# Optimization experiments

Measured on AMD Instinct MI355X. Metric: run time of the kernel, lower is better.

## Reference

```python
import jax, jax.numpy as jnp
import numpy as np

N = 10000   # num_nodes (batch=1)
E = 160000  # num edges
CIN, H, T, OUT, K = 32, 64, 12, 12, 3


def _conv1d(x, w, b, pad):
    # x: [N, C_in, T], w: [C_out, C_in, K]
    out = jax.lax.conv_general_dilated(
        x, w, window_strides=(1,), padding=[(pad, pad)],
        dimension_numbers=('NCH', 'OIH', 'NCH'))
    return out + b[None, :, None]


def _gated_tconv(x, w, b):
    # GatedTemporalConv (dropout = identity in eval)
    out = _conv1d(x, w, b, K // 2)
    P, Q = jnp.split(out, 2, axis=1)
    return P * jax.nn.sigmoid(Q)


def _gcn(x, W, b, src, dst, ew):
    # PyG GCNConv, vectorized over all T timesteps in one fused pass.
    # x: [N, C_in, T], W: [C_out, C_in]
    xt = jnp.einsum('nct,oc->not', x, W)
    loop = jnp.arange(N)
    srcl = jnp.concatenate([src, loop])
    dstl = jnp.concatenate([dst, loop])
    ewl = jnp.concatenate([ew, jnp.ones((N,), ew.dtype)])
    deg = jax.ops.segment_sum(ewl, dstl, num_segments=N)
    dis = jnp.where(deg > 0, jax.lax.rsqrt(deg), 0.0)
    norm = dis[srcl] * ewl * dis[dstl]                      # [E+N]
    msg = xt[srcl] * norm[:, None, None]                    # [E+N, C_out, T]
    out = jax.ops.segment_sum(msg, dstl, num_segments=N)    # [N, C_out, T]
    return out + b[None, :, None]


def setup_inputs() -> dict:
    key = jax.random.key(0)
    ks = jax.random.split(key, 20)
    rn = lambda k, s: jax.random.normal(k, s, jnp.float32) * 0.05
    return {
        'x': jax.random.normal(ks[0], (N, CIN, T), jnp.float32),
        'edge_index': jax.random.randint(ks[1], (2, E), 0, N),
        'edge_weight': jax.random.uniform(ks[2], (E,), jnp.float32),
        'tc1a_w': rn(ks[3], (2 * H, CIN, K)), 'tc1a_b': rn(ks[4], (2 * H,)),
        'gc1_w': rn(ks[5], (H, H)),           'gc1_b': rn(ks[6], (H,)),
        'tc1b_w': rn(ks[7], (2 * H, H, K)),   'tc1b_b': rn(ks[8], (2 * H,)),
        'tc2a_w': rn(ks[9], (2 * H, H, K)),   'tc2a_b': rn(ks[10], (2 * H,)),
        'gc2_w': rn(ks[11], (H, H)),          'gc2_b': rn(ks[12], (H,)),
        'tc2b_w': rn(ks[13], (2 * H, H, K)),  'tc2b_b': rn(ks[14], (2 * H,)),
        'fin_w': rn(ks[15], (OUT, H, T)),     'fin_b': rn(ks[16], (OUT,)),
    }


def reference(x, edge_index, edge_weight,
              tc1a_w, tc1a_b, gc1_w, gc1_b, tc1b_w, tc1b_b,
              tc2a_w, tc2a_b, gc2_w, gc2_b, tc2b_w, tc2b_b,
              fin_w, fin_b):
    src, dst = edge_index[0], edge_index[1]
    h = _gated_tconv(x, tc1a_w, tc1a_b)
    h = jax.nn.relu(_gcn(h, gc1_w, gc1_b, src, dst, edge_weight))
    h = _gated_tconv(h, tc1b_w, tc1b_b)
    h = _gated_tconv(h, tc2a_w, tc2a_b)
    h = jax.nn.relu(_gcn(h, gc2_w, gc2_b, src, dst, edge_weight))
    h = _gated_tconv(h, tc2b_w, tc2b_b)
    h = _conv1d(h, fin_w, fin_b, 0)          # [N, OUT, 1] (kernel == T)
    h = h[:, :, 0]                            # squeeze(-1)
    return h.reshape(1, N, OUT)               # batch_size = 1
```

## Files before the change

### kernel.cpp

```cpp
#include <hip/hip_runtime.h>
#include <hip/hip_bf16.h>
#include <stdint.h>

#define N_NODES 10000
#define N_EDGES 160000
#define BUCKET 128
#define UNROLL_SLOTS 24

typedef unsigned short u16;
typedef unsigned int u32;
typedef short s16v8 __attribute__((ext_vector_type(8)));
typedef float f32v4 __attribute__((ext_vector_type(4)));
typedef float f32v2 __attribute__((ext_vector_type(2)));
typedef unsigned int u32v4 __attribute__((ext_vector_type(4)));
typedef unsigned int u32v2 __attribute__((ext_vector_type(2)));

__device__ __forceinline__ float bf2f(u16 v){ return __uint_as_float(((u32)v) << 16); }
__device__ __forceinline__ u16 f2bf(float f){
    u32 u = __float_as_uint(f);
    u32 r = (u + 0x7fffu + ((u >> 16) & 1u)) >> 16;
    return (u16)r;
}
__device__ __forceinline__ f32v2 up2(u32 v){
    f32v2 r;
    r.x = __uint_as_float(v << 16);
    r.y = __uint_as_float(v & 0xffff0000u);
    return r;
}
__device__ __forceinline__ u32 pk2(float lo, float hi){
    return (u32)f2bf(lo) | ((u32)f2bf(hi) << 16);
}

struct SmallPtrs { const void* p[14]; };

__device__ __constant__ const int g_seg_off[15] = {
    0, 12288, 12416, 16512, 16576, 41152, 41280,
    65856, 65984, 70080, 70144, 94720, 94848, 104064, 104076
};
__device__ __constant__ const int g_seg_kind[14] = {
    1, 0, 0, 0, 2, 0, 2, 0, 0, 0, 2, 0, 0, 0
};

__global__ void k_convert_init(SmallPtrs ps, u16* __restrict__ dst,
                               float* deg, int* cur){
    int i = blockIdx.x * blockDim.x + threadIdx.x;
    if (i < 104076){
        int seg = 0, base = 0;
#pragma unroll
        for (int s = 0; s < 14; s++){
            if (i >= g_seg_off[s]){ seg = s; base = g_seg_off[s]; }
        }
        int li = i - base;
        float v = ((const float*)ps.p[seg])[li];
        int kind = g_seg_kind[seg];
        int dsto = li;
        if (kind){
            int CIN = (kind == 1) ? 32 : 64;
            int o = li / (3 * CIN);
            int rem = li - o * (3 * CIN);
            int c = rem / 3, d = rem - c * 3;
            dsto = d * 128 * CIN + o * CIN + c;
        }
        dst[base + dsto] = f2bf(v);
    }
    if (i < N_NODES){ deg[i] = 1.0f; cur[i] = 0; }
}

__launch_bounds__(256, 4)
__global__ void k_gconv_count(const float* __restrict__ xin, const u16* __restrict__ wg,
                              const u16* __restrict__ bg, u16* __restrict__ out,
                              const int* __restrict__ ei, const float* __restrict__ ew,
                              float* deg, int* cur, int2* __restrict__ epack){
    if (blockIdx.x >= 1250){
        int e = (blockIdx.x - 1250) * 256 + threadIdx.x;
        if (e < N_EDGES){
            int s = ei[e];
            int d = ei[N_EDGES + e];
            float wv = ew[e];
            atomicAdd(&deg[d], wv);
            int p = atomicAdd(&cur[d], 1);
            if (p < BUCKET) epack[d * BUCKET + p] = make_int2(s, __float_as_int(wv));
        }
        return;
    }
    __shared__ __attribute__((aligned(16))) u16 shbuf[6912];
    u16* xT = shbuf;
    u16* Ho = shbuf;
    int tid = threadIdx.x;
    int n0 = blockIdx.x * 8;

    int lane = tid & 63, wave = tid >> 6;
    int col = lane & 15, quad = lane >> 4;
    int o_p = wave * 16 + col, o_q = o_p + 64;

    s16v8 Bf[3][2];
#pragma unroll
    for (int pq = 0; pq < 2; pq++){
        int o = pq ? o_q : o_p;
#pragma unroll
        for (int d = 0; d < 3; d++)
            Bf[d][pq] = *(const s16v8*)(wg + d * 4096 + o * 32 + quad * 8);
    }

    for (int i = tid; i < 8 * 40; i += 256){
        int g = i / 40, c = i % 40;
        xT[g * 560 + 0 * 40 + c] = 0; xT[g * 560 + 13 * 40 + c] = 0;
    }
    {
        int g = tid >> 5, c = tid & 31;
        const float4* p = (const float4*)(xin + ((size_t)(n0 + g) * 32 + c) * 12);
        float4 v0 = p[0], v1 = p[1], v2 = p[2];
        u16* xb = xT + g * 560 + c;
        xb[1 * 40] = f2bf(v0.x);  xb[2 * 40] = f2bf(v0.y);
        xb[3 * 40] = f2bf(v0.z);  xb[4 * 40] = f2bf(v0.w);
        xb[5 * 40] = f2bf(v1.x);  xb[6 * 40] = f2bf(v1.y);
        xb[7 * 40] = f2bf(v1.z);  xb[8 * 40] = f2bf(v1.w);
        xb[9 * 40] = f2bf(v2.x);  xb[10 * 40] = f2bf(v2.y);
        xb[11 * 40] = f2bf(v2.z); xb[12 * 40] = f2bf(v2.w);
    }
    __syncthreads();

    f32v4 aP[6], aQ[6];
#pragma unroll
    for (int mt = 0; mt < 6; mt++){ aP[mt] = (f32v4)0.f; aQ[mt] = (f32v4)0.f; }
#pragma unroll
    for (int mt = 0; mt < 6; mt++){
        int m = mt * 16 + col;
        int g = m / 12, t = m - 12 * g;
#pragma unroll
        for (int d = 0; d < 3; d++){
            s16v8 a = *(const s16v8*)&xT[g * 560 + (t + d) * 40 + quad * 8];
            aP[mt] = __builtin_amdgcn_mfma_f32_16x16x32_bf16(a, Bf[d][0], aP[mt], 0, 0, 0);
            aQ[mt] = __builtin_amdgcn_mfma_f32_16x16x32_bf16(a, Bf[d][1], aQ[mt], 0, 0, 0);
        }
    }
    __syncthreads();
    float bP = bf2f(bg[o_p]), bQ = bf2f(bg[o_q]);
#pragma unroll
    for (int mt = 0; mt < 6; mt++){
#pragma unroll
        for (int r = 0; r < 4; r++){
            int m2 = mt * 16 + quad * 4 + r;
            int g = m2 / 12, t = m2 - 12 * g;
            float pv = aP[mt][r] + bP, qv = aQ[mt][r] + bQ;
            Ho[g * 864 + t * 72 + o_p] = f2bf(pv / (1.f + __expf(-qv)));
        }
    }
    __syncthreads();
    for (int i = tid; i < 768; i += 256){
        int g = i / 96, r = i % 96, t = r / 8, ch = r % 8;
        *(s16v8*)(out + (size_t)(n0 + g) * 768 + t * 64 + ch * 8) =
            *(const s16v8*)&Ho[g * 864 + t * 72 + ch * 8];
    }
}

__global__ void k_norm(const float* __restrict__ deg, const int* __restrict__ cur,
                       int2* __restrict__ ep){
    int i = blockIdx.x * blockDim.x + threadIdx.x;
    int n = i >> 7, slot = i & 127;
    if (n >= N_NODES) return;
    int cnt = cur[n]; if (cnt > BUCKET) cnt = BUCKET;
    if (slot < cnt){
        int2 e = ep[(size_t)n * BUCKET + slot];
        float w = __int_as_float(e.y) * rsqrtf(deg[e.x]) * rsqrtf(deg[n]);
        ep[(size_t)n * BUCKET + slot].y = __float_as_int(w);
    } else if (slot < UNROLL_SLOTS){
        ep[(size_t)n * BUCKET + slot] = make_int2(0, 0);
    }
}

#define GATHER2(P) { \
    int4 m = *(const int4*)(eb + (P)); \
    const u16* q0 = src + (size_t)(u32)m.x * 768; \
    const u16* q1 = src + (size_t)(u32)m.z * 768; \
    u32v4 a0 = *(const u32v4*)(q0 + off1); u32v2 b0 = *(const u32v2*)(q0 + off2); \
    u32v4 a1 = *(const u32v4*)(q1 + off1); u32v2 b1 = *(const u32v2*)(q1 + off2); \
    f32v2 w0; w0.x = __int_as_float(m.y); w0.y = w0.x; \
    f32v2 w1; w1.x = __int_as_float(m.w); w1.y = w1.x; \
    acc[0] += w0 * up2(a0.x); acc[1] += w0 * up2(a0.y); \
    acc[2] += w0 * up2(a0.z); acc[3] += w0 * up2(a0.w); \
    acc[4] += w0 * up2(b0.x); acc[5] += w0 * up2(b0.y); \
    acc[0] += w1 * up2(a1.x); acc[1] += w1 * up2(a1.y); \
    acc[2] += w1 * up2(a1.z); acc[3] += w1 * up2(a1.w); \
    acc[4] += w1 * up2(b1.x); acc[5] += w1 * up2(b1.y); }

#define GATHER1(P) { \
    int2 e0 = eb[(P)]; \
    const u16* q0 = src + (size_t)(u32)e0.x * 768; \
    u32v4 a0 = *(const u32v4*)(q0 + off1); u32v2 b0 = *(const u32v2*)(q0 + off2); \
    f32v2 w0; w0.x = __int_as_float(e0.y); w0.y = w0.x; \
    acc[0] += w0 * up2(a0.x); acc[1] += w0 * up2(a0.y); \
    acc[2] += w0 * up2(a0.z); acc[3] += w0 * up2(a0.w); \
    acc[4] += w0 * up2(b0.x); acc[5] += w0 * up2(b0.y); }

__launch_bounds__(256, 8)
__global__ void k_gather(const u16* __restrict__ src, const float* __restrict__ deg,
                         const int* __restrict__ cur, const int2* __restrict__ ep,
                         u16* __restrict__ z){
    int slice = blockIdx.x & 7;
    int nb = blockIdx.x >> 3;
    int tid = threadIdx.x;
    int nl = tid >> 5;
    int sub = tid & 31;
    int eg = sub >> 3;
    int l8 = sub & 7;
    int n = nb * 8 + nl;
    int off1 = slice * 96 + l8 * 8;
    int off2 = slice * 96 + 64 + l8 * 4;

    int e = cur[n]; if (e > BUCKET) e = BUCKET;

    f32v2 acc[6];
    if (eg == 0){
        float sw = 1.0f / deg[n];
        f32v2 swv; swv.x = sw; swv.y = sw;
        const u16* xr = src + (size_t)n * 768;
        u32v4 sa = *(const u32v4*)(xr + off1);
        u32v2 sb = *(const u32v2*)(xr + off2);
        acc[0] = swv * up2(sa.x); acc[1] = swv * up2(sa.y);
        acc[2] = swv * up2(sa.z); acc[3] = swv * up2(sa.w);
        acc[4] = swv * up2(sb.x); acc[5] = swv * up2(sb.y);
    } else {
#pragma unroll
        for (int k = 0; k < 6; k++) acc[k] = (f32v2)0.f;
    }

    const int2* eb = ep + (size_t)n * BUCKET;
    GATHER2(eg * 2);
    GATHER2(eg * 2 + 8);
    GATHER2(eg * 2 + 16);

    if (e > UNROLL_SLOTS){
        int p = UNROLL_SLOTS + eg * 2;
        for (; p + 1 < e; p += 8) GATHER2(p);
        if (p < e) GATHER1(p);
    }

    float r[12];
#pragma unroll
    for (int j = 0; j < 6; j++){ r[2 * j] = acc[j].x; r[2 * j + 1] = acc[j].y; }
#pragma unroll
    for (int k = 0; k < 12; k++){
        r[k] += __shfl_xor(r[k], 8, 64);
        r[k] += __shfl_xor(r[k], 16, 64);
    }
    if (eg == 0){
        u16* zo = z + (size_t)n * 768;
        u32v4 ha; ha.x = pk2(r[0], r[1]); ha.y = pk2(r[2], r[3]);
        ha.z = pk2(r[4], r[5]); ha.w = pk2(r[6], r[7]);
        u32v2 hb; hb.x = pk2(r[8], r[9]); hb.y = pk2(r[10], r[11]);
        *(u32v4*)(zo + off1) = ha;
        *(u32v2*)(zo + off2) = hb;
    }
}

#define XIDX(g, row, c) (((g) * 14 + (row)) * 72 + (c))

template<bool LAST>
__launch_bounds__(256, 4)
__global__ void k_fused(const u16* __restrict__ z,
                        const u16* __restrict__ Wmix, const u16* __restrict__ bmix,
                        const u16* __restrict__ w1, const u16* __restrict__ b1,
                        const u16* __restrict__ w2, const u16* __restrict__ b2,
                        const u16* __restrict__ fw, const u16* __restrict__ fb,
                        u16* __restrict__ outMid, float* __restrict__ outFin){
    __shared__ __attribute__((aligned(16))) u16 bufX[8 * 14 * 72];
    __shared__ __attribute__((aligned(16))) u16 bufY[8 * 14 * 72];
    int tid = threadIdx.x;
    int n0 = blockIdx.x * 8;
    int lane = tid & 63, wave = tid >> 6;
    int col = lane & 15, quad = lane >> 4;
    int o_p = wave * 16 + col, o_q = o_p + 64;

    for (int i = tid; i < 8 * 72; i += 256){
        int g = i / 72, c = i % 72;
        bufX[XIDX(g, 0, c)] = 0; bufX[XIDX(g, 13, c)] = 0;
        bufY[XIDX(g, 0, c)] = 0; bufY[XIDX(g, 13, c)] = 0;
    }
    for (int i = tid; i < 768; i += 256){
        int g = i / 96, r = i % 96, t = r >> 3, ch = r & 7;
        *(s16v8*)&bufX[XIDX(g, 1 + t, ch * 8)] =
            *(const s16v8*)(z + (size_t)(n0 + g) * 768 + t * 64 + ch * 8);
    }
    __syncthreads();

    {
        f32v4 accm[6];
#pragma unroll
        for (int mt = 0; mt < 6; mt++) accm[mt] = (f32v4)0.f;
#pragma unroll
        for (int ks = 0; ks < 2; ks++){
            s16v8 Bm = *(const s16v8*)(Wmix + (size_t)o_p * 64 + ks * 32 + quad * 8);
#pragma unroll
            for (int mt = 0; mt < 6; mt++){
                int m = mt * 16 + col;
                int g = m / 12, t = m - 12 * g;
                s16v8 a = *(const s16v8*)&bufX[XIDX(g, 1 + t, ks * 32 + quad * 8)];
                accm[mt] = __builtin_amdgcn_mfma_f32_16x16x32_bf16(a, Bm, accm[mt], 0, 0, 0);
            }
        }
        float bm = bf2f(bmix[o_p]);
#pragma unroll
        for (int mt = 0; mt < 6; mt++){
#pragma unroll
            for (int r = 0; r < 4; r++){
                int m2 = mt * 16 + quad * 4 + r;
                int g = m2 / 12, t = m2 - 12 * g;
                bufY[XIDX(g, 1 + t, o_p)] = f2bf(fmaxf(accm[mt][r] + bm, 0.f));
            }
        }
    }
    __syncthreads();

    {
        f32v4 aP[6], aQ[6];
#pragma unroll
        for (int mt = 0; mt < 6; mt++){ aP[mt] = (f32v4)0.f; aQ[mt] = (f32v4)0.f; }
#pragma unroll
        for (int ks = 0; ks < 2; ks++){
            s16v8 Bf[3][2];
#pragma unroll
            for (int pq = 0; pq < 2; pq++){
                int o = pq ? o_q : o_p;
#pragma unroll
                for (int d = 0; d < 3; d++)
                    Bf[d][pq] = *(const s16v8*)(w1 + d * 8192 + o * 64 + ks * 32 + quad * 8);
            }
#pragma unroll
            for (int mt = 0; mt < 6; mt++){
                int m = mt * 16 + col;
                int g = m / 12, t = m - 12 * g;
#pragma unroll
                for (int d = 0; d < 3; d++){
                    s16v8 a = *(const s16v8*)&bufY[XIDX(g, t + d, ks * 32 + quad * 8)];
                    aP[mt] = __builtin_amdgcn_mfma_f32_16x16x32_bf16(a, Bf[d][0], aP[mt], 0, 0, 0);
                    aQ[mt] = __builtin_amdgcn_mfma_f32_16x16x32_bf16(a, Bf[d][1], aQ[mt], 0, 0, 0);
                }
            }
        }
        float bP = bf2f(b1[o_p]), bQ = bf2f(b1[o_q]);
#pragma unroll
        for (int mt = 0; mt < 6; mt++){
#pragma unroll
            for (int r = 0; r < 4; r++){
                int m2 = mt * 16 + quad * 4 + r;
                int g = m2 / 12, t = m2 - 12 * g;
                float pv = aP[mt][r] + bP, qv = aQ[mt][r] + bQ;
                u16 hv = f2bf(pv / (1.f + __expf(-qv)));
                if (LAST) bufX[g * 1008 + o_p * 12 + t] = hv;
                else      bufX[XIDX(g, 1 + t, o_p)] = hv;
            }
        }
    }
    __syncthreads();

    if (!LAST){
        f32v4 aP[6], aQ[6];
#pragma unroll
        for (int mt = 0; mt < 6; mt++){ aP[mt] = (f32v4)0.f; aQ[mt] = (f32v4)0.f; }
#pragma unroll
        for (int ks = 0; ks < 2; ks++){
            s16v8 Bf[3][2];
#pragma unroll
            for (int pq = 0; pq < 2; pq++){
                int o = pq ? o_q : o_p;
#pragma unroll
                for (int d = 0; d < 3; d++)
                    Bf[d][pq] = *(const s16v8*)(w2 + d * 8192 + o * 64 + ks * 32 + quad * 8);
            }
#pragma unroll
            for (int mt = 0; mt < 6; mt++){
                int m = mt * 16 + col;
                int g = m / 12, t = m - 12 * g;
#pragma unroll
                for (int d = 0; d < 3; d++){
                    s16v8 a = *(const s16v8*)&bufX[XIDX(g, t + d, ks * 32 + quad * 8)];
                    aP[mt] = __builtin_amdgcn_mfma_f32_16x16x32_bf16(a, Bf[d][0], aP[mt], 0, 0, 0);
                    aQ[mt] = __builtin_amdgcn_mfma_f32_16x16x32_bf16(a, Bf[d][1], aQ[mt], 0, 0, 0);
                }
            }
        }
        float bP = bf2f(b2[o_p]), bQ = bf2f(b2[o_q]);
#pragma unroll
        for (int mt = 0; mt < 6; mt++){
#pragma unroll
            for (int r = 0; r < 4; r++){
                int m2 = mt * 16 + quad * 4 + r;
                int g = m2 / 12, t = m2 - 12 * g;
                float pv = aP[mt][r] + bP, qv = aQ[mt][r] + bQ;
                bufY[XIDX(g, 1 + t, o_p)] = f2bf(pv / (1.f + __expf(-qv)));
            }
        }
        __syncthreads();
        for (int i = tid; i < 768; i += 256){
            int g = i / 96, r = i % 96, t = r / 8, ch = r % 8;
            *(s16v8*)(outMid + (size_t)(n0 + g) * 768 + t * 64 + ch * 8) =
                *(const s16v8*)&bufY[XIDX(g, 1 + t, ch * 8)];
        }
    } else {
        if (wave == 0){
            f32v4 accF = {0.f, 0.f, 0.f, 0.f};
            int g8 = col & 7;
#pragma unroll
            for (int ks = 0; ks < 24; ks++){
                s16v8 a = *(const s16v8*)&bufX[g8 * 1008 + ks * 32 + quad * 8];
                s16v8 bfr = {0, 0, 0, 0, 0, 0, 0, 0};
                if (col < 12)
                    bfr = *(const s16v8*)(fw + (size_t)col * 768 + ks * 32 + quad * 8);
                accF = __builtin_amdgcn_mfma_f32_16x16x32_bf16(a, bfr, accF, 0, 0, 0);
            }
            if (col < 12 && quad < 2){
                float bb = bf2f(fb[col]);
#pragma unroll
                for (int r = 0; r < 4; r++){
                    int g = quad * 4 + r;
                    outFin[(size_t)(n0 + g) * 12 + col] = accF[r] + bb;
                }
            }
        }
    }
}

static inline size_t align256(size_t x){ return (x + 255) & ~(size_t)255; }

extern "C" void kernel_launch(void* const* d_in, const int* in_sizes, int n_in,
                              void* d_out, int out_size, void* d_ws, size_t ws_size,
                              hipStream_t stream){
    const float* x  = (const float*)d_in[0];
    const int* ei   = (const int*)d_in[1];
    const float* ew = (const float*)d_in[2];

    char* w = (char*)d_ws;
    u16* bufA    = (u16*)w;  w += align256((size_t)N_NODES * 768 * sizeof(u16));
    u16* bufB    = (u16*)w;  w += align256((size_t)N_NODES * 768 * sizeof(u16));
    u16* zA      = (u16*)w;  w += align256((size_t)N_NODES * 768 * sizeof(u16));
    u16* zB      = (u16*)w;  w += align256((size_t)N_NODES * 768 * sizeof(u16));
    float* deg   = (float*)w; w += align256(N_NODES * sizeof(float));
    int* cur     = (int*)w;   w += align256(N_NODES * sizeof(int));
    int2* epack  = (int2*)w;  w += align256((size_t)N_NODES * BUCKET * sizeof(int2));
    u16* cvt     = (u16*)w;   w += align256(104076 * sizeof(u16));

    u16* tc1a_w = cvt + 0;
    u16* tc1a_b = cvt + 12288;
    u16* gc1_w  = cvt + 12416;
    u16* gc1_b  = cvt + 16512;
    u16* tc1b_w = cvt + 16576;
    u16* tc1b_b = cvt + 41152;
    u16* tc2a_w = cvt + 41280;
    u16* tc2a_b = cvt + 65856;
    u16* gc2_w  = cvt + 65984;
    u16* gc2_b  = cvt + 70080;
    u16* tc2b_w = cvt + 70144;
    u16* tc2b_b = cvt + 94720;
    u16* fin_w  = cvt + 94848;
    u16* fin_b  = cvt + 104064;

    SmallPtrs ps;
    ps.p[0]  = d_in[3];  ps.p[1]  = d_in[4];
    ps.p[2]  = d_in[5];  ps.p[3]  = d_in[6];
    ps.p[4]  = d_in[7];  ps.p[5]  = d_in[8];
    ps.p[6]  = d_in[9];  ps.p[7]  = d_in[10];
    ps.p[8]  = d_in[11]; ps.p[9]  = d_in[12];
    ps.p[10] = d_in[13]; ps.p[11] = d_in[14];
    ps.p[12] = d_in[15]; ps.p[13] = d_in[16];

    k_convert_init<<<(104076 + 255) / 256, 256, 0, stream>>>(ps, cvt, deg, cur);
    k_gconv_count<<<1250 + 625, 256, 0, stream>>>(x, tc1a_w, tc1a_b, bufA, ei, ew, deg, cur, epack);
    k_norm<<<(N_NODES * BUCKET) / 256, 256, 0, stream>>>(deg, cur, epack);

    k_gather<<<1250 * 8, 256, 0, stream>>>(bufA, deg, cur, epack, zA);
    k_fused<false><<<1250, 256, 0, stream>>>(zA, gc1_w, gc1_b, tc1b_w, tc1b_b,
                                             tc2a_w, tc2a_b, nullptr, nullptr,
                                             bufB, nullptr);
    k_gather<<<1250 * 8, 256, 0, stream>>>(bufB, deg, cur, epack, zB);
    k_fused<true><<<1250, 256, 0, stream>>>(zB, gc2_w, gc2_b, tc2b_w, tc2b_b,
                                            nullptr, nullptr, fin_w, fin_b,
                                            nullptr, (float*)d_out);
}
```

Measured before the change: 226.7 us.

## Fuse graph gather aggregation into the fused conv kernel

Removes the separate k_gather kernels and performs the normalized neighbor aggregation inside the fused mix/temporal-conv kernel, writing results straight into shared memory. This eliminates the round-trip of the z intermediate through global memory and two kernel launches. In exchange, each thread now processes one node's full 768-feature row across 24 accumulators with serial edge iteration, and the gather is spread over 1250 blocks instead of 10000. That reduces parallelism and latency hiding for the irregular, random-access gather and raises register pressure.

```diff
diff --git a/kernel.cpp b/kernel.cpp
--- a/kernel.cpp
+++ b/kernel.cpp
@@ -169,101 +169,50 @@
     }
 }
 
-#define GATHER2(P) { \
+#define XIDX(g, row, c) (((g) * 14 + (row)) * 72 + (c))
+
+#define GFMA(W, A0, A1, A2) { \
+    acc[0]  += (W) * up2((A0).x); acc[1]  += (W) * up2((A0).y); \
+    acc[2]  += (W) * up2((A0).z); acc[3]  += (W) * up2((A0).w); \
+    acc[4]  += (W) * up2((A1).x); acc[5]  += (W) * up2((A1).y); \
+    acc[6]  += (W) * up2((A1).z); acc[7]  += (W) * up2((A1).w); \
+    acc[8]  += (W) * up2((A2).x); acc[9]  += (W) * up2((A2).y); \
+    acc[10] += (W) * up2((A2).z); acc[11] += (W) * up2((A2).w); }
+
+#define GPAIR(P) { \
     int4 m = *(const int4*)(eb + (P)); \
-    const u16* q0 = src + (size_t)(u32)m.x * 768; \
-    const u16* q1 = src + (size_t)(u32)m.z * 768; \
-    u32v4 a0 = *(const u32v4*)(q0 + off1); u32v2 b0 = *(const u32v2*)(q0 + off2); \
-    u32v4 a1 = *(const u32v4*)(q1 + off1); u32v2 b1 = *(const u32v2*)(q1 + off2); \
+    const u16* q0 = src + (size_t)(u32)m.x * 768 + fo; \
+    const u16* q1 = src + (size_t)(u32)m.z * 768 + fo; \
+    u32v4 a0 = *(const u32v4*)(q0); \
+    u32v4 a1 = *(const u32v4*)(q0 + 256); \
+    u32v4 a2 = *(const u32v4*)(q0 + 512); \
+    u32v4 c0 = *(const u32v4*)(q1); \
+    u32v4 c1 = *(const u32v4*)(q1 + 256); \
+    u32v4 c2 = *(const u32v4*)(q1 + 512); \
     f32v2 w0; w0.x = __int_as_float(m.y); w0.y = w0.x; \
     f32v2 w1; w1.x = __int_as_float(m.w); w1.y = w1.x; \
-    acc[0] += w0 * up2(a0.x); acc[1] += w0 * up2(a0.y); \
-    acc[2] += w0 * up2(a0.z); acc[3] += w0 * up2(a0.w); \
-    acc[4] += w0 * up2(b0.x); acc[5] += w0 * up2(b0.y); \
-    acc[0] += w1 * up2(a1.x); acc[1] += w1 * up2(a1.y); \
-    acc[2] += w1 * up2(a1.z); acc[3] += w1 * up2(a1.w); \
-    acc[4] += w1 * up2(b1.x); acc[5] += w1 * up2(b1.y); }
-
-#define GATHER1(P) { \
+    GFMA(w0, a0, a1, a2); \
+    GFMA(w1, c0, c1, c2); }
+
+#define GSINGLE(P) { \
     int2 e0 = eb[(P)]; \
-    const u16* q0 = src + (size_t)(u32)e0.x * 768; \
-    u32v4 a0 = *(const u32v4*)(q0 + off1); u32v2 b0 = *(const u32v2*)(q0 + off2); \
+    const u16* q0 = src + (size_t)(u32)e0.x * 768 + fo; \
+    u32v4 a0 = *(const u32v4*)(q0); \
+    u32v4 a1 = *(const u32v4*)(q0 + 256); \
+    u32v4 a2 = *(const u32v4*)(q0 + 512); \
     f32v2 w0; w0.x = __int_as_float(e0.y); w0.y = w0.x; \
-    acc[0] += w0 * up2(a0.x); acc[1] += w0 * up2(a0.y); \
-    acc[2] += w0 * up2(a0.z); acc[3] += w0 * up2(a0.w); \
-    acc[4] += w0 * up2(b0.x); acc[5] += w0 * up2(b0.y); }
-
-__launch_bounds__(256, 8)
-__global__ void k_gather(const u16* __restrict__ src, const float* __restrict__ deg,
-                         const int* __restrict__ cur, const int2* __restrict__ ep,
-                         u16* __restrict__ z){
-    int slice = blockIdx.x & 7;
-    int nb = blockIdx.x >> 3;
-    int tid = threadIdx.x;
-    int nl = tid >> 5;
-    int sub = tid & 31;
-    int eg = sub >> 3;
-    int l8 = sub & 7;
-    int n = nb * 8 + nl;
-    int off1 = slice * 96 + l8 * 8;
-    int off2 = slice * 96 + 64 + l8 * 4;
-
-    int e = cur[n]; if (e > BUCKET) e = BUCKET;
-
-    f32v2 acc[6];
-    if (eg == 0){
-        float sw = 1.0f / deg[n];
-        f32v2 swv; swv.x = sw; swv.y = sw;
-        const u16* xr = src + (size_t)n * 768;
-        u32v4 sa = *(const u32v4*)(xr + off1);
-        u32v2 sb = *(const u32v2*)(xr + off2);
-        acc[0] = swv * up2(sa.x); acc[1] = swv * up2(sa.y);
-        acc[2] = swv * up2(sa.z); acc[3] = swv * up2(sa.w);
-        acc[4] = swv * up2(sb.x); acc[5] = swv * up2(sb.y);
-    } else {
-#pragma unroll
-        for (int k = 0; k < 6; k++) acc[k] = (f32v2)0.f;
-    }
-
-    const int2* eb = ep + (size_t)n * BUCKET;
-    GATHER2(eg * 2);
-    GATHER2(eg * 2 + 8);
-    GATHER2(eg * 2 + 16);
-
-    if (e > UNROLL_SLOTS){
-        int p = UNROLL_SLOTS + eg * 2;
-        for (; p + 1 < e; p += 8) GATHER2(p);
-        if (p < e) GATHER1(p);
-    }
-
-    float r[12];
-#pragma unroll
-    for (int j = 0; j < 6; j++){ r[2 * j] = acc[j].x; r[2 * j + 1] = acc[j].y; }
-#pragma unroll
-    for (int k = 0; k < 12; k++){
-        r[k] += __shfl_xor(r[k], 8, 64);
-        r[k] += __shfl_xor(r[k], 16, 64);
-    }
-    if (eg == 0){
-        u16* zo = z + (size_t)n * 768;
-        u32v4 ha; ha.x = pk2(r[0], r[1]); ha.y = pk2(r[2], r[3]);
-        ha.z = pk2(r[4], r[5]); ha.w = pk2(r[6], r[7]);
-        u32v2 hb; hb.x = pk2(r[8], r[9]); hb.y = pk2(r[10], r[11]);
-        *(u32v4*)(zo + off1) = ha;
-        *(u32v2*)(zo + off2) = hb;
-    }
-}
-
-#define XIDX(g, row, c) (((g) * 14 + (row)) * 72 + (c))
+    GFMA(w0, a0, a1, a2); }
 
 template<bool LAST>
 __launch_bounds__(256, 4)
-__global__ void k_fused(const u16* __restrict__ z,
-                        const u16* __restrict__ Wmix, const u16* __restrict__ bmix,
-                        const u16* __restrict__ w1, const u16* __restrict__ b1,
-                        const u16* __restrict__ w2, const u16* __restrict__ b2,
-                        const u16* __restrict__ fw, const u16* __restrict__ fb,
-                        u16* __restrict__ outMid, float* __restrict__ outFin){
+__global__ void k_gfused(const u16* __restrict__ src,
+                         const float* __restrict__ deg, const int* __restrict__ cur,
+                         const int2* __restrict__ ep,
+                         const u16* __restrict__ Wmix, const u16* __restrict__ bmix,
+                         const u16* __restrict__ w1, const u16* __restrict__ b1,
+                         const u16* __restrict__ w2, const u16* __restrict__ b2,
+                         const u16* __restrict__ fw, const u16* __restrict__ fb,
+                         u16* __restrict__ outMid, float* __restrict__ outFin){
     __shared__ __attribute__((aligned(16))) u16 bufX[8 * 14 * 72];
     __shared__ __attribute__((aligned(16))) u16 bufY[8 * 14 * 72];
     int tid = threadIdx.x;
@@ -277,10 +226,52 @@
         bufX[XIDX(g, 0, c)] = 0; bufX[XIDX(g, 13, c)] = 0;
         bufY[XIDX(g, 0, c)] = 0; bufY[XIDX(g, 13, c)] = 0;
     }
-    for (int i = tid; i < 768; i += 256){
-        int g = i / 96, r = i % 96, t = r >> 3, ch = r & 7;
-        *(s16v8*)&bufX[XIDX(g, 1 + t, ch * 8)] =
-            *(const s16v8*)(z + (size_t)(n0 + g) * 768 + t * 64 + ch * 8);
+
+    {
+        int nl = tid >> 5;
+        int l  = tid & 31;
+        int n  = n0 + nl;
+        int fo = l * 8;
+        int e = cur[n]; if (e > BUCKET) e = BUCKET;
+
+        f32v2 acc[12];
+        {
+            float sw = 1.0f / deg[n];
+            f32v2 swv; swv.x = sw; swv.y = sw;
+            const u16* q = src + (size_t)n * 768 + fo;
+            u32v4 s0 = *(const u32v4*)(q);
+            u32v4 s1 = *(const u32v4*)(q + 256);
+            u32v4 s2 = *(const u32v4*)(q + 512);
+            acc[0]  = swv * up2(s0.x); acc[1]  = swv * up2(s0.y);
+            acc[2]  = swv * up2(s0.z); acc[3]  = swv * up2(s0.w);
+            acc[4]  = swv * up2(s1.x); acc[5]  = swv * up2(s1.y);
+            acc[6]  = swv * up2(s1.z); acc[7]  = swv * up2(s1.w);
+            acc[8]  = swv * up2(s2.x); acc[9]  = swv * up2(s2.y);
+            acc[10] = swv * up2(s2.z); acc[11] = swv * up2(s2.w);
+        }
+
+        const int2* eb = ep + (size_t)n * BUCKET;
+        GPAIR(0);  GPAIR(2);  GPAIR(4);  GPAIR(6);
+        GPAIR(8);  GPAIR(10); GPAIR(12); GPAIR(14);
+        GPAIR(16); GPAIR(18); GPAIR(20); GPAIR(22);
+
+        if (e > UNROLL_SLOTS){
+            int p = UNROLL_SLOTS;
+            for (; p + 1 < e; p += 2) GPAIR(p);
+            if (p < e) GSINGLE(p);
+        }
+
+#pragma unroll
+        for (int gi = 0; gi < 3; gi++){
+            int f0 = gi * 256 + fo;
+            int t = f0 >> 6, c = f0 & 63;
+            u32v4 hv;
+            hv.x = pk2(acc[4 * gi + 0].x, acc[4 * gi + 0].y);
+            hv.y = pk2(acc[4 * gi + 1].x, acc[4 * gi + 1].y);
+            hv.z = pk2(acc[4 * gi + 2].x, acc[4 * gi + 2].y);
+            hv.w = pk2(acc[4 * gi + 3].x, acc[4 * gi + 3].y);
+            *(u32v4*)&bufX[XIDX(nl, 1 + t, c)] = hv;
+        }
     }
     __syncthreads();
 
@@ -433,8 +424,6 @@
     char* w = (char*)d_ws;
     u16* bufA    = (u16*)w;  w += align256((size_t)N_NODES * 768 * sizeof(u16));
     u16* bufB    = (u16*)w;  w += align256((size_t)N_NODES * 768 * sizeof(u16));
-    u16* zA      = (u16*)w;  w += align256((size_t)N_NODES * 768 * sizeof(u16));
-    u16* zB      = (u16*)w;  w += align256((size_t)N_NODES * 768 * sizeof(u16));
     float* deg   = (float*)w; w += align256(N_NODES * sizeof(float));
     int* cur     = (int*)w;   w += align256(N_NODES * sizeof(int));
     int2* epack  = (int2*)w;  w += align256((size_t)N_NODES * BUCKET * sizeof(int2));
@@ -468,12 +457,12 @@
     k_gconv_count<<<1250 + 625, 256, 0, stream>>>(x, tc1a_w, tc1a_b, bufA, ei, ew, deg, cur, epack);
     k_norm<<<(N_NODES * BUCKET) / 256, 256, 0, stream>>>(deg, cur, epack);
 
-    k_gather<<<1250 * 8, 256, 0, stream>>>(bufA, deg, cur, epack, zA);
-    k_fused<false><<<1250, 256, 0, stream>>>(zA, gc1_w, gc1_b, tc1b_w, tc1b_b,
-                                             tc2a_w, tc2a_b, nullptr, nullptr,
-                                             bufB, nullptr);
-    k_gather<<<1250 * 8, 256, 0, stream>>>(bufB, deg, cur, epack, zB);
-    k_fused<true><<<1250, 256, 0, stream>>>(zB, gc2_w, gc2_b, tc2b_w, tc2b_b,
-                                            nullptr, nullptr, fin_w, fin_b,
-                                            nullptr, (float*)d_out);
-}
+    k_gfused<false><<<1250, 256, 0, stream>>>(bufA, deg, cur, epack,
+                                              gc1_w, gc1_b, tc1b_w, tc1b_b,
+                                              tc2a_w, tc2a_b, nullptr, nullptr,
+                                              bufB, nullptr);
+    k_gfused<true><<<1250, 256, 0, stream>>>(bufB, deg, cur, epack,
+                                             gc2_w, gc2_b, tc2b_w, tc2b_b,
+                                             nullptr, nullptr, fin_w, fin_b,
+                                             nullptr, (float*)d_out);
+}
```

Result: no change. 225.4 us (-0.6%).
